# Optimization experiments

Hardware: AMD Instinct MI355X
Metric: run time of the kernel (lower is better)

Reference implementation:

```python
import jax, jax.numpy as jnp
import numpy as np

B, S, D_IN, D_H = 4, 2048, 1024, 1024

def setup_inputs() -> dict:
    key = jax.random.key(0)
    k1, k2, k3, k4 = jax.random.split(key, 4)
    x = jax.random.normal(k1, (B, S, D_IN), dtype=jnp.float32)
    # torch nn.Linear weights are [out, in]; kept in that layout
    Wq = jax.random.normal(k2, (D_H, D_IN), dtype=jnp.float32) * (1.0 / np.sqrt(D_IN))
    Wk = jax.random.normal(k3, (D_H, D_IN), dtype=jnp.float32) * (1.0 / np.sqrt(D_IN))
    Wv = jax.random.normal(k4, (D_H, D_IN), dtype=jnp.float32) * (1.0 / np.sqrt(D_IN))
    return {"x": x, "Wq": Wq, "Wk": Wk, "Wv": Wv}

def reference(x, Wq, Wk, Wv):
    # projections (Linear, no bias): x @ W.T
    q = jnp.einsum('bsd,hd->bsh', x, Wq)
    k = jnp.einsum('bsd,hd->bsh', x, Wk)
    v = jnp.einsum('bsd,hd->bsh', x, Wv)
    scores = jnp.einsum('bqh,bkh->bqk', q, k)  # [B,S,S]
    S_len = x.shape[1]
    causal = jnp.triu(jnp.ones((S_len, S_len), dtype=bool), k=1)
    scores = jnp.where(causal, -jnp.inf, scores) / jnp.sqrt(jnp.float32(k.shape[-1]))
    attn = jax.nn.softmax(scores, axis=-1)
    # dropout is identity in eval/deterministic mode
    return jnp.einsum('bqk,bkh->bqh', attn, v)
```

## Files before the change

### kernel.cpp

```cpp
#include <hip/hip_runtime.h>
#include <hip/hip_bf16.h>
#include <stdint.h>

typedef unsigned short u16;
typedef __attribute__((ext_vector_type(8))) short short8;
typedef __attribute__((ext_vector_type(4))) float f32x4;
typedef __attribute__((ext_vector_type(4))) u16 u16x4;

#define S_LEN 2048
#define D_DIM 1024
#define NBATCH 4
#define BM 128
#define BN 128
#define BK 32

enum { MODE_QKV = 0, MODE_SC = 2, MODE_PV = 3 };

__device__ inline u16 f2bf(float f) {
  uint32_t u = __float_as_uint(f);
  uint32_t r = (u + 0x7fffu + ((u >> 16) & 1u)) >> 16;
  return (u16)r;
}

__global__ __launch_bounds__(256) void cast_f32_bf16(
    const float* __restrict__ in, u16* __restrict__ out, int n) {
  int i = (blockIdx.x * blockDim.x + threadIdx.x) * 4;
  int stride = gridDim.x * blockDim.x * 4;
  for (; i < n; i += stride) {
    f32x4 v = *reinterpret_cast<const f32x4*>(in + i);
    u16x4 o;
    o[0] = f2bf(v[0]); o[1] = f2bf(v[1]); o[2] = f2bf(v[2]); o[3] = f2bf(v[3]);
    *reinterpret_cast<u16x4*>(out + i) = o;
  }
}

template <int MODE>
__global__ __launch_bounds__(256, 2) void gemm_bt(
    const u16* __restrict__ A, const u16* __restrict__ B, void* __restrict__ C,
    int K, long strideAb, long strideBb, long strideCb, int ldc,
    float* __restrict__ aux) {
  __shared__ u16 As[2][BM * BK];
  __shared__ u16 Bs[2][BN * BK];

  const int bz = blockIdx.z;
  const u16* Ab = A + (long)bz * strideAb;
  const u16* Bb = B + (long)bz * strideBb;

  int br, bc;
  if (MODE == MODE_SC) {
    int t = blockIdx.x;
    int r = (int)((sqrtf(8.0f * (float)t + 1.0f) - 1.0f) * 0.5f);
    while ((r + 1) * (r + 2) / 2 <= t) ++r;
    while (r * (r + 1) / 2 > t) --r;
    br = r;
    bc = t - r * (r + 1) / 2;
  } else if (MODE == MODE_PV) {
    int xr = blockIdx.x;
    int nt = gridDim.x;
    br = (xr & 1) ? (xr >> 1) : (nt - 1 - (xr >> 1));
    bc = blockIdx.y;
  } else {
    int lin = blockIdx.y * gridDim.x + blockIdx.x;
    int nwg = gridDim.x * gridDim.y;
    int cpx = nwg >> 3;
    int swz = (lin & 7) * cpx + (lin >> 3);
    br = swz % gridDim.x;
    bc = swz / gridDim.x;
  }

  const int rowBase = br * BM;
  const int colBase = bc * BN;
  int nkt = (MODE == MODE_PV) ? (br + 1) * (BM / BK) : (K / BK);

  const int tid = threadIdx.x;
  const int lane = tid & 63;
  const int wave = tid >> 6;
  const int wr = wave >> 1, wc = wave & 1;

  f32x4 acc[4][4];
#pragma unroll
  for (int i = 0; i < 4; i++)
#pragma unroll
    for (int j = 0; j < 4; j++) acc[i][j] = f32x4{0.f, 0.f, 0.f, 0.f};

  const int srow = tid >> 2;
  const int skc = (tid & 3) * 8;

  auto stage = [&](int buf, int kt) {
    const u16* ga = Ab + (long)(rowBase + srow) * K + kt * BK + skc;
    const u16* gb = Bb + (long)(colBase + srow) * K + kt * BK + skc;
    __builtin_amdgcn_global_load_lds(
        (const __attribute__((address_space(1))) void*)ga,
        (__attribute__((address_space(3))) void*)(&As[buf][tid * 8]), 16, 0, 0);
    __builtin_amdgcn_global_load_lds(
        (const __attribute__((address_space(1))) void*)(ga + (long)64 * K),
        (__attribute__((address_space(3))) void*)(&As[buf][64 * BK + tid * 8]), 16, 0, 0);
    __builtin_amdgcn_global_load_lds(
        (const __attribute__((address_space(1))) void*)gb,
        (__attribute__((address_space(3))) void*)(&Bs[buf][tid * 8]), 16, 0, 0);
    __builtin_amdgcn_global_load_lds(
        (const __attribute__((address_space(1))) void*)(gb + (long)64 * K),
        (__attribute__((address_space(3))) void*)(&Bs[buf][64 * BK + tid * 8]), 16, 0, 0);
  };

  stage(0, 0);
  int cur = 0;
  for (int kt = 0; kt < nkt; ++kt) {
    if (kt + 1 < nkt) stage(cur ^ 1, kt + 1);
    __syncthreads();
    short8 af[4], bf[4];
#pragma unroll
    for (int i = 0; i < 4; i++)
      af[i] = *reinterpret_cast<const short8*>(
          &As[cur][(wr * 64 + i * 16 + (lane & 15)) * BK + (lane >> 4) * 8]);
#pragma unroll
    for (int j = 0; j < 4; j++)
      bf[j] = *reinterpret_cast<const short8*>(
          &Bs[cur][(wc * 64 + j * 16 + (lane & 15)) * BK + (lane >> 4) * 8]);
#pragma unroll
    for (int i = 0; i < 4; i++)
#pragma unroll
      for (int j = 0; j < 4; j++)
        acc[i][j] = __builtin_amdgcn_mfma_f32_16x16x32_bf16(af[i], bf[j], acc[i][j], 0, 0, 0);
    __syncthreads();
    cur ^= 1;
  }

  const int lr = (lane >> 4) * 4;
  const int lc = lane & 15;

  if (MODE == MODE_QKV) {
    u16* Cb = (u16*)C;
    const long seg = (long)NBATCH * S_LEN * D_DIM;
    const int segi = colBase >> 10;
    const int hb = colBase & 1023;
    if (segi < 2) {
      u16* dst = Cb + (long)segi * seg;
#pragma unroll
      for (int i = 0; i < 4; i++) {
        int r0 = rowBase + wr * 64 + i * 16 + lr;
#pragma unroll
        for (int j = 0; j < 4; j++) {
          int c0 = hb + wc * 64 + j * 16 + lc;
#pragma unroll
          for (int q = 0; q < 4; q++) dst[(long)(r0 + q) * D_DIM + c0] = f2bf(acc[i][j][q]);
        }
      }
    } else {
      u16* dst = Cb + 2 * seg;
#pragma unroll
      for (int i = 0; i < 4; i++) {
        int m0 = rowBase + wr * 64 + i * 16 + lr;
        int b = m0 >> 11, s0 = m0 & (S_LEN - 1);
#pragma unroll
        for (int j = 0; j < 4; j++) {
          int h = hb + wc * 64 + j * 16 + lc;
          u16x4 o;
          o[0] = f2bf(acc[i][j][0]); o[1] = f2bf(acc[i][j][1]);
          o[2] = f2bf(acc[i][j][2]); o[3] = f2bf(acc[i][j][3]);
          *reinterpret_cast<u16x4*>(dst + ((long)b * D_DIM + h) * S_LEN + s0) = o;
        }
      }
    }
  } else if (MODE == MODE_SC) {
    u16* Cb = (u16*)C + (long)bz * strideCb;
    float* lp = aux + (long)bz * S_LEN * 32;
#pragma unroll
    for (int i = 0; i < 4; i++) {
      int r0 = rowBase + wr * 64 + i * 16 + lr;
#pragma unroll
      for (int q = 0; q < 4; q++) {
        int r = r0 + q;
        float rs = 0.f;
#pragma unroll
        for (int j = 0; j < 4; j++) {
          int c0 = colBase + wc * 64 + j * 16 + lc;
          float p = (c0 <= r) ? __expf(acc[i][j][q] * 0.03125f - 8.f) : 0.f;
          rs += p;
          Cb[(long)r * ldc + c0] = f2bf(p);
        }
#pragma unroll
        for (int off = 1; off < 16; off <<= 1) rs += __shfl_xor(rs, off);
        if ((lane & 15) == 0) lp[r * 32 + bc * 2 + wc] = rs;
      }
    }
  } else {
    float* Cb = (float*)C + (long)bz * strideCb;
    const float* il = aux + (long)bz * S_LEN;
#pragma unroll
    for (int i = 0; i < 4; i++) {
      int r0 = rowBase + wr * 64 + i * 16 + lr;
#pragma unroll
      for (int j = 0; j < 4; j++) {
        int c0 = colBase + wc * 64 + j * 16 + lc;
#pragma unroll
        for (int q = 0; q < 4; q++)
          Cb[(long)(r0 + q) * ldc + c0] = acc[i][j][q] * il[r0 + q];
      }
    }
  }
}

__global__ __launch_bounds__(256) void row_inv(
    const float* __restrict__ lp, float* __restrict__ il, int nrows) {
  int r = blockIdx.x * blockDim.x + threadIdx.x;
  if (r < nrows) {
    const float* p = lp + (long)r * 32;
    float s = 0.f;
#pragma unroll
    for (int k = 0; k < 32; k += 4) {
      f32x4 v = *reinterpret_cast<const f32x4*>(p + k);
      s += v[0] + v[1] + v[2] + v[3];
    }
    il[r] = 1.f / s;
  }
}

extern "C" void kernel_launch(void* const* d_in, const int* in_sizes, int n_in,
                              void* d_out, int out_size, void* d_ws, size_t ws_size,
                              hipStream_t stream) {
  const float* x = (const float*)d_in[0];
  const float* Wq = (const float*)d_in[1];
  const float* Wk = (const float*)d_in[2];
  const float* Wv = (const float*)d_in[3];
  float* out = (float*)d_out;

  const size_t SD = (size_t)S_LEN * D_DIM;
  const size_t SS = (size_t)S_LEN * S_LEN;
  const size_t DD = (size_t)D_DIM * D_DIM;

  size_t off = 0;
  char* ws = (char*)d_ws;
  auto alloc = [&](size_t bytes) -> char* {
    char* p = ws + off;
    off += (bytes + 255) & ~(size_t)255;
    return p;
  };
  u16* xb = (u16*)alloc(NBATCH * SD * 2);
  u16* Wqkvb = (u16*)alloc(3 * DD * 2);
  u16* QKVt = (u16*)alloc(3 * NBATCH * SD * 2);
  u16* Qb = QKVt;
  u16* Kb = QKVt + NBATCH * SD;
  u16* Vt = QKVt + 2 * NBATCH * SD;
  size_t base_off = off;
  size_t need_full = base_off + ((NBATCH * SS * 2 + 255) & ~(size_t)255) +
                     ((NBATCH * (size_t)S_LEN * 32 * 4 + 255) & ~(size_t)255) +
                     ((NBATCH * (size_t)S_LEN * 4 + 255) & ~(size_t)255);
  const int nbpar = (ws_size >= need_full) ? NBATCH : 1;
  u16* P = (u16*)alloc((size_t)nbpar * SS * 2);
  float* l_part = (float*)alloc((size_t)nbpar * S_LEN * 32 * 4);
  float* inv_l = (float*)alloc((size_t)nbpar * S_LEN * 4);

  cast_f32_bf16<<<2048, 256, 0, stream>>>(x, xb, (int)(NBATCH * SD));
  cast_f32_bf16<<<512, 256, 0, stream>>>(Wq, Wqkvb, (int)DD);
  cast_f32_bf16<<<512, 256, 0, stream>>>(Wk, Wqkvb + DD, (int)DD);
  cast_f32_bf16<<<512, 256, 0, stream>>>(Wv, Wqkvb + 2 * DD, (int)DD);

  dim3 gp((NBATCH * S_LEN) / BM, 3 * D_DIM / BN, 1);
  gemm_bt<MODE_QKV><<<gp, 256, 0, stream>>>(xb, Wqkvb, QKVt, D_DIM, 0, 0, 0, D_DIM, nullptr);

  const int ntri = (S_LEN / BM) * (S_LEN / BM + 1) / 2;
  if (nbpar == NBATCH) {
    hipMemsetAsync(l_part, 0, (size_t)NBATCH * S_LEN * 32 * 4, stream);
    gemm_bt<MODE_SC><<<dim3(ntri, 1, NBATCH), 256, 0, stream>>>(
        Qb, Kb, P, D_DIM, (long)SD, (long)SD, (long)SS, S_LEN, l_part);
    row_inv<<<dim3(NBATCH * S_LEN / 256), 256, 0, stream>>>(l_part, inv_l, NBATCH * S_LEN);
    gemm_bt<MODE_PV><<<dim3(S_LEN / BM, D_DIM / BN, NBATCH), 256, 0, stream>>>(
        P, Vt, out, S_LEN, (long)SS, (long)SD, (long)SD, D_DIM, inv_l);
  } else {
    for (int b = 0; b < NBATCH; ++b) {
      hipMemsetAsync(l_part, 0, (size_t)S_LEN * 32 * 4, stream);
      gemm_bt<MODE_SC><<<dim3(ntri, 1, 1), 256, 0, stream>>>(
          Qb + b * SD, Kb + b * SD, P, D_DIM, 0, 0, 0, S_LEN, l_part);
      row_inv<<<dim3(S_LEN / 256), 256, 0, stream>>>(l_part, inv_l, S_LEN);
      gemm_bt<MODE_PV><<<dim3(S_LEN / BM, D_DIM / BN, 1), 256, 0, stream>>>(
          P, Vt + b * SD, out + b * SD, S_LEN, 0, 0, 0, D_DIM, inv_l);
    }
  }
}
```

Baseline: 186.0 us.

## Use 256x256 QKV GEMM tiles, fuse casts, fold row normalization into PV

```diff
diff --git a/kernel.cpp b/kernel.cpp
--- a/kernel.cpp
+++ b/kernel.cpp
@@ -14,7 +14,7 @@
 #define BN 128
 #define BK 32
 
-enum { MODE_QKV = 0, MODE_SC = 2, MODE_PV = 3 };
+enum { MODE_SC = 2, MODE_PV = 3 };
 
 __device__ inline u16 f2bf(float f) {
   uint32_t u = __float_as_uint(f);
@@ -22,15 +22,130 @@
   return (u16)r;
 }
 
-__global__ __launch_bounds__(256) void cast_f32_bf16(
-    const float* __restrict__ in, u16* __restrict__ out, int n) {
-  int i = (blockIdx.x * blockDim.x + threadIdx.x) * 4;
-  int stride = gridDim.x * blockDim.x * 4;
-  for (; i < n; i += stride) {
-    f32x4 v = *reinterpret_cast<const f32x4*>(in + i);
+__global__ __launch_bounds__(256) void cast_all(
+    const float* __restrict__ x, const float* __restrict__ wq,
+    const float* __restrict__ wk, const float* __restrict__ wv,
+    u16* __restrict__ out) {
+  const int X4 = (NBATCH * S_LEN * D_DIM) / 4;
+  const int W4 = (D_DIM * D_DIM) / 4;
+  const int total = X4 + 3 * W4;
+  int g = blockIdx.x * blockDim.x + threadIdx.x;
+  int stride = gridDim.x * blockDim.x;
+  for (; g < total; g += stride) {
+    const float* src;
+    int si;
+    if (g < X4) { src = x; si = g; }
+    else if (g < X4 + W4) { src = wq; si = g - X4; }
+    else if (g < X4 + 2 * W4) { src = wk; si = g - X4 - W4; }
+    else { src = wv; si = g - X4 - 2 * W4; }
+    f32x4 v = *reinterpret_cast<const f32x4*>(src + (long)si * 4);
     u16x4 o;
     o[0] = f2bf(v[0]); o[1] = f2bf(v[1]); o[2] = f2bf(v[2]); o[3] = f2bf(v[3]);
-    *reinterpret_cast<u16x4*>(out + i) = o;
+    *reinterpret_cast<u16x4*>(out + (long)g * 4) = o;
+  }
+}
+
+__global__ __launch_bounds__(512, 2) void gemm_qkv256(
+    const u16* __restrict__ A, const u16* __restrict__ B, u16* __restrict__ C, int K) {
+  __shared__ u16 As[2][256 * BK];
+  __shared__ u16 Bs[2][256 * BK];
+
+  int lin = blockIdx.y * gridDim.x + blockIdx.x;
+  int cpx = (gridDim.x * gridDim.y) >> 3;
+  int swz = (lin & 7) * cpx + (lin >> 3);
+  const int br = swz % gridDim.x;
+  const int bc = swz / gridDim.x;
+  const int rowBase = br * 256;
+  const int colBase = bc * 256;
+
+  const int tid = threadIdx.x;
+  const int lane = tid & 63;
+  const int wave = tid >> 6;
+  const int wr = wave >> 2;
+  const int wc = wave & 3;
+  const int l15 = lane & 15;
+  const int g = lane >> 4;
+
+  f32x4 acc[8][4];
+#pragma unroll
+  for (int i = 0; i < 8; i++)
+#pragma unroll
+    for (int j = 0; j < 4; j++) acc[i][j] = f32x4{0.f, 0.f, 0.f, 0.f};
+
+  const int srow = tid >> 2;
+  const int slot = (tid & 3) * 8;
+
+  auto stage = [&](int buf, int kt) {
+#pragma unroll
+    for (int s = 0; s < 2; ++s) {
+      const u16* ga = A + (long)(rowBase + s * 128 + srow) * K + kt * BK + slot;
+      const u16* gb = B + (long)(colBase + s * 128 + srow) * K + kt * BK + slot;
+      __builtin_amdgcn_global_load_lds(
+          (const __attribute__((address_space(1))) void*)ga,
+          (__attribute__((address_space(3))) void*)(&As[buf][s * 128 * BK + tid * 8]),
+          16, 0, 0);
+      __builtin_amdgcn_global_load_lds(
+          (const __attribute__((address_space(1))) void*)gb,
+          (__attribute__((address_space(3))) void*)(&Bs[buf][s * 128 * BK + tid * 8]),
+          16, 0, 0);
+    }
+  };
+
+  const int nkt = K / BK;
+  stage(0, 0);
+  int cur = 0;
+  for (int kt = 0; kt < nkt; ++kt) {
+    if (kt + 1 < nkt) stage(cur ^ 1, kt + 1);
+    __syncthreads();
+    short8 af[8], bf[4];
+#pragma unroll
+    for (int i = 0; i < 8; i++)
+      af[i] = *reinterpret_cast<const short8*>(
+          &As[cur][(wr * 128 + i * 16 + l15) * BK + g * 8]);
+#pragma unroll
+    for (int j = 0; j < 4; j++)
+      bf[j] = *reinterpret_cast<const short8*>(
+          &Bs[cur][(wc * 64 + j * 16 + l15) * BK + g * 8]);
+#pragma unroll
+    for (int i = 0; i < 8; i++)
+#pragma unroll
+      for (int j = 0; j < 4; j++)
+        acc[i][j] = __builtin_amdgcn_mfma_f32_16x16x32_bf16(af[i], bf[j], acc[i][j], 0, 0, 0);
+    __syncthreads();
+    cur ^= 1;
+  }
+
+  const int lr = g * 4;
+  const long seg = (long)NBATCH * S_LEN * D_DIM;
+  const int segi = colBase >> 10;
+  const int hb = colBase & 1023;
+  if (segi < 2) {
+    u16* dst = C + (long)segi * seg;
+#pragma unroll
+    for (int i = 0; i < 8; i++) {
+      int r0 = rowBase + wr * 128 + i * 16 + lr;
+#pragma unroll
+      for (int j = 0; j < 4; j++) {
+        int c0 = hb + wc * 64 + j * 16 + l15;
+#pragma unroll
+        for (int q = 0; q < 4; q++) dst[(long)(r0 + q) * D_DIM + c0] = f2bf(acc[i][j][q]);
+      }
+    }
+  } else {
+    u16* dst = C + 2 * seg;
+#pragma unroll
+    for (int i = 0; i < 8; i++) {
+      int m0 = rowBase + wr * 128 + i * 16 + lr;
+      int b = m0 >> 11, s0 = m0 & (S_LEN - 1);
+#pragma unroll
+      for (int j = 0; j < 4; j++) {
+        int h = hb + wc * 64 + j * 16 + l15;
+        u16x4 o;
+        o[0] = f2bf(acc[i][j][0]); o[1] = f2bf(acc[i][j][1]);
+        o[2] = f2bf(acc[i][j][2]); o[3] = f2bf(acc[i][j][3]);
+        *reinterpret_cast<u16x4*>(dst + ((long)b * D_DIM + h) * S_LEN + s0) = o;
+      }
+    }
   }
 }
 
@@ -41,6 +156,7 @@
     float* __restrict__ aux) {
   __shared__ u16 As[2][BM * BK];
   __shared__ u16 Bs[2][BN * BK];
+  __shared__ float ilds[BM];
 
   const int bz = blockIdx.z;
   const u16* Ab = A + (long)bz * strideAb;
@@ -54,18 +170,11 @@
     while (r * (r + 1) / 2 > t) --r;
     br = r;
     bc = t - r * (r + 1) / 2;
-  } else if (MODE == MODE_PV) {
+  } else {
     int xr = blockIdx.x;
     int nt = gridDim.x;
     br = (xr & 1) ? (xr >> 1) : (nt - 1 - (xr >> 1));
     bc = blockIdx.y;
-  } else {
-    int lin = blockIdx.y * gridDim.x + blockIdx.x;
-    int nwg = gridDim.x * gridDim.y;
-    int cpx = nwg >> 3;
-    int swz = (lin & 7) * cpx + (lin >> 3);
-    br = swz % gridDim.x;
-    bc = swz / gridDim.x;
   }
 
   const int rowBase = br * BM;
@@ -76,6 +185,14 @@
   const int lane = tid & 63;
   const int wave = tid >> 6;
   const int wr = wave >> 1, wc = wave & 1;
+
+  if (MODE == MODE_PV && tid < BM) {
+    const float* lp = aux + (long)bz * S_LEN * 32 + (long)(rowBase + tid) * 32;
+    float s = 0.f;
+    int nslot = 2 * (br + 1);
+    for (int k = 0; k < nslot; ++k) s += lp[k];
+    ilds[tid] = 1.f / s;
+  }
 
   f32x4 acc[4][4];
 #pragma unroll
@@ -129,40 +246,7 @@
   const int lr = (lane >> 4) * 4;
   const int lc = lane & 15;
 
-  if (MODE == MODE_QKV) {
-    u16* Cb = (u16*)C;
-    const long seg = (long)NBATCH * S_LEN * D_DIM;
-    const int segi = colBase >> 10;
-    const int hb = colBase & 1023;
-    if (segi < 2) {
-      u16* dst = Cb + (long)segi * seg;
-#pragma unroll
-      for (int i = 0; i < 4; i++) {
-        int r0 = rowBase + wr * 64 + i * 16 + lr;
-#pragma unroll
-        for (int j = 0; j < 4; j++) {
-          int c0 = hb + wc * 64 + j * 16 + lc;
-#pragma unroll
-          for (int q = 0; q < 4; q++) dst[(long)(r0 + q) * D_DIM + c0] = f2bf(acc[i][j][q]);
-        }
-      }
-    } else {
-      u16* dst = Cb + 2 * seg;
-#pragma unroll
-      for (int i = 0; i < 4; i++) {
-        int m0 = rowBase + wr * 64 + i * 16 + lr;
-        int b = m0 >> 11, s0 = m0 & (S_LEN - 1);
-#pragma unroll
-        for (int j = 0; j < 4; j++) {
-          int h = hb + wc * 64 + j * 16 + lc;
-          u16x4 o;
-          o[0] = f2bf(acc[i][j][0]); o[1] = f2bf(acc[i][j][1]);
-          o[2] = f2bf(acc[i][j][2]); o[3] = f2bf(acc[i][j][3]);
-          *reinterpret_cast<u16x4*>(dst + ((long)b * D_DIM + h) * S_LEN + s0) = o;
-        }
-      }
-    }
-  } else if (MODE == MODE_SC) {
+  if (MODE == MODE_SC) {
     u16* Cb = (u16*)C + (long)bz * strideCb;
     float* lp = aux + (long)bz * S_LEN * 32;
 #pragma unroll
@@ -186,7 +270,6 @@
     }
   } else {
     float* Cb = (float*)C + (long)bz * strideCb;
-    const float* il = aux + (long)bz * S_LEN;
 #pragma unroll
     for (int i = 0; i < 4; i++) {
       int r0 = rowBase + wr * 64 + i * 16 + lr;
@@ -195,24 +278,9 @@
         int c0 = colBase + wc * 64 + j * 16 + lc;
 #pragma unroll
         for (int q = 0; q < 4; q++)
-          Cb[(long)(r0 + q) * ldc + c0] = acc[i][j][q] * il[r0 + q];
+          Cb[(long)(r0 + q) * ldc + c0] = acc[i][j][q] * ilds[wr * 64 + i * 16 + lr + q];
       }
     }
-  }
-}
-
-__global__ __launch_bounds__(256) void row_inv(
-    const float* __restrict__ lp, float* __restrict__ il, int nrows) {
-  int r = blockIdx.x * blockDim.x + threadIdx.x;
-  if (r < nrows) {
-    const float* p = lp + (long)r * 32;
-    float s = 0.f;
-#pragma unroll
-    for (int k = 0; k < 32; k += 4) {
-      f32x4 v = *reinterpret_cast<const f32x4*>(p + k);
-      s += v[0] + v[1] + v[2] + v[3];
-    }
-    il[r] = 1.f / s;
   }
 }
 
@@ -236,45 +304,36 @@
     off += (bytes + 255) & ~(size_t)255;
     return p;
   };
-  u16* xb = (u16*)alloc(NBATCH * SD * 2);
-  u16* Wqkvb = (u16*)alloc(3 * DD * 2);
+  u16* xb = (u16*)alloc((NBATCH * SD + 3 * DD) * 2);
+  u16* Wqkvb = xb + NBATCH * SD;
   u16* QKVt = (u16*)alloc(3 * NBATCH * SD * 2);
   u16* Qb = QKVt;
   u16* Kb = QKVt + NBATCH * SD;
   u16* Vt = QKVt + 2 * NBATCH * SD;
   size_t base_off = off;
   size_t need_full = base_off + ((NBATCH * SS * 2 + 255) & ~(size_t)255) +
-                     ((NBATCH * (size_t)S_LEN * 32 * 4 + 255) & ~(size_t)255) +
-                     ((NBATCH * (size_t)S_LEN * 4 + 255) & ~(size_t)255);
+                     ((NBATCH * (size_t)S_LEN * 32 * 4 + 255) & ~(size_t)255);
   const int nbpar = (ws_size >= need_full) ? NBATCH : 1;
   u16* P = (u16*)alloc((size_t)nbpar * SS * 2);
   float* l_part = (float*)alloc((size_t)nbpar * S_LEN * 32 * 4);
-  float* inv_l = (float*)alloc((size_t)nbpar * S_LEN * 4);
-
-  cast_f32_bf16<<<2048, 256, 0, stream>>>(x, xb, (int)(NBATCH * SD));
-  cast_f32_bf16<<<512, 256, 0, stream>>>(Wq, Wqkvb, (int)DD);
-  cast_f32_bf16<<<512, 256, 0, stream>>>(Wk, Wqkvb + DD, (int)DD);
-  cast_f32_bf16<<<512, 256, 0, stream>>>(Wv, Wqkvb + 2 * DD, (int)DD);
-
-  dim3 gp((NBATCH * S_LEN) / BM, 3 * D_DIM / BN, 1);
-  gemm_bt<MODE_QKV><<<gp, 256, 0, stream>>>(xb, Wqkvb, QKVt, D_DIM, 0, 0, 0, D_DIM, nullptr);
+
+  cast_all<<<2048, 256, 0, stream>>>(x, Wq, Wk, Wv, xb);
+
+  dim3 g256((NBATCH * S_LEN) / 256, (3 * D_DIM) / 256, 1);
+  gemm_qkv256<<<g256, 512, 0, stream>>>(xb, Wqkvb, QKVt, D_DIM);
 
   const int ntri = (S_LEN / BM) * (S_LEN / BM + 1) / 2;
   if (nbpar == NBATCH) {
-    hipMemsetAsync(l_part, 0, (size_t)NBATCH * S_LEN * 32 * 4, stream);
     gemm_bt<MODE_SC><<<dim3(ntri, 1, NBATCH), 256, 0, stream>>>(
         Qb, Kb, P, D_DIM, (long)SD, (long)SD, (long)SS, S_LEN, l_part);
-    row_inv<<<dim3(NBATCH * S_LEN / 256), 256, 0, stream>>>(l_part, inv_l, NBATCH * S_LEN);
     gemm_bt<MODE_PV><<<dim3(S_LEN / BM, D_DIM / BN, NBATCH), 256, 0, stream>>>(
-        P, Vt, out, S_LEN, (long)SS, (long)SD, (long)SD, D_DIM, inv_l);
+        P, Vt, out, S_LEN, (long)SS, (long)SD, (long)SD, D_DIM, l_part);
   } else {
     for (int b = 0; b < NBATCH; ++b) {
-      hipMemsetAsync(l_part, 0, (size_t)S_LEN * 32 * 4, stream);
       gemm_bt<MODE_SC><<<dim3(ntri, 1, 1), 256, 0, stream>>>(
           Qb + b * SD, Kb + b * SD, P, D_DIM, 0, 0, 0, S_LEN, l_part);
-      row_inv<<<dim3(S_LEN / 256), 256, 0, stream>>>(l_part, inv_l, S_LEN);
       gemm_bt<MODE_PV><<<dim3(S_LEN / BM, D_DIM / BN, 1), 256, 0, stream>>>(
-          P, Vt + b * SD, out + b * SD, S_LEN, 0, 0, 0, D_DIM, inv_l);
-    }
-  }
-}
+          P, Vt + b * SD, out + b * SD, S_LEN, 0, 0, 0, D_DIM, l_part);
+    }
+  }
+}
```

New measurement: 204.6 us. 10.0% more time.
